# Kernel optimization log

Measured on AMD Instinct MI355X. Metric: run time of the kernel, lower is better.

## Reference

```python
import jax, jax.numpy as jnp
import numpy as np

DIM = 1024
HEADS = 16
HD = DIM // HEADS  # 64
EPS = 1.1920928955078125e-07  # torch.finfo(float32).eps, RMSNorm default


def setup_inputs() -> dict:
    key = jax.random.key(0)
    ks = jax.random.split(key, 8)
    s = 0.02
    return {
        "x": jax.random.normal(ks[0], (2, 2048, DIM), jnp.float32),
        "pe": jax.random.normal(ks[1], (1, 1, 2048, HD // 2, 2, 2), jnp.float32),
        "qkv_w": jax.random.normal(ks[2], (3 * DIM, DIM), jnp.float32) * s,
        "qkv_b": jax.random.normal(ks[3], (3 * DIM,), jnp.float32) * s,
        "q_norm_w": jnp.ones((HD,), jnp.float32),
        "k_norm_w": jnp.ones((HD,), jnp.float32),
        "proj_w": jax.random.normal(ks[4], (DIM, DIM), jnp.float32) * s,
        "proj_b": jax.random.normal(ks[5], (DIM,), jnp.float32) * s,
    }


def _rms_norm(t, w):
    var = jnp.mean(jnp.square(t), axis=-1, keepdims=True)
    return t * jax.lax.rsqrt(var + EPS) * w


def _apply_rope(t, pe):
    # t: [B,H,L,D]; pe: [1,1,L,D/2,2,2]
    B, H, L, D = t.shape
    tp = t.reshape(B, H, L, D // 2, 1, 2)
    out = pe[..., 0] * tp[..., 0] + pe[..., 1] * tp[..., 1]  # [B,H,L,D/2,2]
    return out.reshape(B, H, L, D)


def reference(x, pe, qkv_w, qkv_b, q_norm_w, k_norm_w, proj_w, proj_b):
    B, L, _ = x.shape
    qkv = x @ qkv_w.T + qkv_b  # [B,L,3*DIM]
    qkv = qkv.reshape(B, L, 3, HEADS, HD).transpose(2, 0, 3, 1, 4)  # [3,B,H,L,D]
    q, k, v = qkv[0], qkv[1], qkv[2]
    q = _rms_norm(q, q_norm_w)
    k = _rms_norm(k, k_norm_w)
    q = _apply_rope(q, pe)
    k = _apply_rope(k, pe)
    scale = 1.0 / np.sqrt(HD).astype(np.float32)
    scores = jnp.einsum("bhqd,bhkd->bhqk", q, k) * scale  # [B,H,L,L]
    attn = jax.nn.softmax(scores, axis=-1)
    o = jnp.einsum("bhqk,bhkd->bhqd", attn, v)  # [B,H,L,D]
    o = o.transpose(0, 2, 1, 3).reshape(B, L, DIM)  # B L (H D)
    return o @ proj_w.T + proj_b
```

## Files before the change

kernel.cpp:

```cpp
#include <hip/hip_runtime.h>
#include <hip/hip_bf16.h>

#define DIM   1024
#define HEADS 16
#define HD    64
#define BB    2
#define LL    2048
#define MTOT  (BB*LL)
#define EPSV  1.1920928955078125e-07f

typedef __attribute__((ext_vector_type(8))) short bf16x8;
typedef __attribute__((ext_vector_type(4))) float f32x4;
typedef unsigned short ushort_t;

__device__ __forceinline__ float bf2f(ushort_t u) {
    unsigned int x = ((unsigned int)u) << 16;
    return __builtin_bit_cast(float, x);
}
__device__ __forceinline__ ushort_t f2bf(float f) {
    unsigned int x = __builtin_bit_cast(unsigned int, f);
    unsigned int r = (x + 0x7FFFu + ((x >> 16) & 1u)) >> 16;
    return (ushort_t)r;
}

__global__ __launch_bounds__(256) void f32_to_bf16_k(const float* __restrict__ in,
                                                     ushort_t* __restrict__ out, int n) {
    int i = (blockIdx.x * 256 + threadIdx.x) * 4;
    if (i < n) {
        float4 v = *(const float4*)(in + i);
        ushort4 o;
        o.x = f2bf(v.x); o.y = f2bf(v.y); o.z = f2bf(v.z); o.w = f2bf(v.w);
        *(ushort4*)(out + i) = o;
    }
}

template <int OUT_BF16>
__global__ __launch_bounds__(256) void gemm_bt(const ushort_t* __restrict__ A,
                                               const ushort_t* __restrict__ Bt,
                                               const float* __restrict__ bias,
                                               void* __restrict__ Cout,
                                               int M, int N, int K) {
    __shared__ __attribute__((aligned(16))) ushort_t Asm[128 * 32];
    __shared__ __attribute__((aligned(16))) ushort_t Bsm[128 * 32];
    int tid = threadIdx.x;
    int lane = tid & 63, wid = tid >> 6;
    int wm = wid >> 1, wn = wid & 1;
    int r = lane & 15, g = lane >> 4;
    int m0 = blockIdx.y * 128, n0 = blockIdx.x * 128;

    f32x4 acc[4][4] = {};

    int niter = K >> 5;
    for (int kk = 0; kk < niter; ++kk) {
        int k0 = kk << 5;
        __syncthreads();
#pragma unroll
        for (int p = 0; p < 2; ++p) {
            int off = (p * 256 + tid) * 8;
            int row = off >> 5, col = off & 31;
            int ldsoff = (p * 256 + wid * 64) * 8;
            __builtin_amdgcn_global_load_lds(
                (const __attribute__((address_space(1))) void*)(A + (size_t)(m0 + row) * K + k0 + col),
                (__attribute__((address_space(3))) void*)(Asm + ldsoff), 16, 0, 0);
            __builtin_amdgcn_global_load_lds(
                (const __attribute__((address_space(1))) void*)(Bt + (size_t)(n0 + row) * K + k0 + col),
                (__attribute__((address_space(3))) void*)(Bsm + ldsoff), 16, 0, 0);
        }
        __syncthreads();
        bf16x8 af[4], bfr[4];
#pragma unroll
        for (int mi = 0; mi < 4; mi++)
            af[mi] = *(const bf16x8*)(Asm + (wm * 64 + mi * 16 + r) * 32 + g * 8);
#pragma unroll
        for (int ni = 0; ni < 4; ni++)
            bfr[ni] = *(const bf16x8*)(Bsm + (wn * 64 + ni * 16 + r) * 32 + g * 8);
#pragma unroll
        for (int mi = 0; mi < 4; mi++)
#pragma unroll
            for (int ni = 0; ni < 4; ni++)
                acc[mi][ni] = __builtin_amdgcn_mfma_f32_16x16x32_bf16(af[mi], bfr[ni], acc[mi][ni], 0, 0, 0);
    }
#pragma unroll
    for (int mi = 0; mi < 4; mi++)
#pragma unroll
        for (int ni = 0; ni < 4; ni++) {
            int col = n0 + wn * 64 + ni * 16 + r;
            float bv = bias[col];
#pragma unroll
            for (int reg = 0; reg < 4; reg++) {
                int row = m0 + wm * 64 + mi * 16 + g * 4 + reg;
                float v = acc[mi][ni][reg] + bv;
                if (OUT_BF16)
                    ((ushort_t*)Cout)[(size_t)row * N + col] = f2bf(v);
                else
                    ((float*)Cout)[(size_t)row * N + col] = v;
            }
        }
}

__global__ __launch_bounds__(256) void norm_rope_k(const ushort_t* __restrict__ qkv,
                                                   const float* __restrict__ pe,
                                                   const float* __restrict__ qnw,
                                                   const float* __restrict__ knw,
                                                   ushort_t* __restrict__ qh,
                                                   ushort_t* __restrict__ kh,
                                                   ushort_t* __restrict__ vT) {
    __shared__ ushort_t T[64][68];
    const int tid = threadIdx.x;
    const int lane = tid & 63, w = tid >> 6;
    const int rg = lane >> 4;
    const int d4 = (lane & 15) * 4;
    const int l0 = blockIdx.x * 64;
    const int t  = blockIdx.y;
    const int bh = blockIdx.z;
    const int b = bh >> 4, h = bh & 15;

    if (t == 2) {
#pragma unroll
        for (int i = 0; i < 4; ++i) {
            int ll = w * 16 + rg + 4 * i;
            int m = b * 2048 + l0 + ll;
            ushort4 v = *(const ushort4*)(qkv + (size_t)m * 3072 + 2048 + h * 64 + d4);
            *(ushort4*)(&T[ll][d4]) = v;
        }
        __syncthreads();
        const int d = tid >> 2, lq = (tid & 3) * 16;
        ushort_t* dst = vT + ((size_t)(bh * 64 + d)) * 2048 + l0 + lq;
#pragma unroll
        for (int c = 0; c < 4; ++c) {
            ushort4 o;
            o.x = T[lq + c * 4 + 0][d];
            o.y = T[lq + c * 4 + 1][d];
            o.z = T[lq + c * 4 + 2][d];
            o.w = T[lq + c * 4 + 3][d];
            *(ushort4*)(dst + c * 4) = o;
        }
        return;
    }

    const float* nwp = (t == 0) ? qnw : knw;
    const float4 nwv = *(const float4*)(nwp + d4);
    ushort_t* dst = (t == 0) ? qh : kh;
    const float qscale = (t == 0) ? 0.125f : 1.0f;
#pragma unroll
    for (int i = 0; i < 4; ++i) {
        int ll = w * 16 + rg + 4 * i;
        int l = l0 + ll;
        int m = b * 2048 + l;
        ushort4 vv = *(const ushort4*)(qkv + (size_t)m * 3072 + t * 1024 + h * 64 + d4);
        float v0 = bf2f(vv.x), v1 = bf2f(vv.y), v2 = bf2f(vv.z), v3 = bf2f(vv.w);
        float ss = v0 * v0 + v1 * v1 + v2 * v2 + v3 * v3;
        ss += __shfl_xor(ss, 1, 64);
        ss += __shfl_xor(ss, 2, 64);
        ss += __shfl_xor(ss, 4, 64);
        ss += __shfl_xor(ss, 8, 64);
        float rms = rsqrtf(ss * (1.0f / 64.0f) + EPSV);
        v0 *= rms * nwv.x; v1 *= rms * nwv.y; v2 *= rms * nwv.z; v3 *= rms * nwv.w;
        float4 p0 = *(const float4*)(pe + (size_t)l * 128 + 2 * d4);
        float4 p1 = *(const float4*)(pe + (size_t)l * 128 + 2 * d4 + 4);
        float o0 = (p0.x * v0 + p0.y * v1) * qscale;
        float o1 = (p0.z * v0 + p0.w * v1) * qscale;
        float o2 = (p1.x * v2 + p1.y * v3) * qscale;
        float o3 = (p1.z * v2 + p1.w * v3) * qscale;
        ushort4 o;
        o.x = f2bf(o0); o.y = f2bf(o1); o.z = f2bf(o2); o.w = f2bf(o3);
        *(ushort4*)(dst + ((size_t)bh * 2048 + l) * 64 + d4) = o;
    }
}

__global__ __launch_bounds__(256, 2) void attn_k(const ushort_t* __restrict__ qh,
                                                 const ushort_t* __restrict__ kh,
                                                 const ushort_t* __restrict__ vT,
                                                 ushort_t* __restrict__ ob) {
    __shared__ __attribute__((aligned(16))) ushort_t Ksm[2][64 * 64];
    __shared__ __attribute__((aligned(16))) ushort_t Vsm[2][64 * 64];
    __shared__ __attribute__((aligned(16))) ushort_t Plds[4][2][16 * 64];

    const int tid = threadIdx.x;
    const int lane = tid & 63, wid = tid >> 6;
    const int r = lane & 15, g = lane >> 4;
    const int qt = blockIdx.x, bh = blockIdx.y;
    const int q0 = qt * 128 + wid * 32;
    const ushort_t* Q  = qh + (size_t)bh * LL * 64;
    const ushort_t* Kb = kh + (size_t)bh * LL * 64;
    const ushort_t* Vt = vT + (size_t)bh * 64 * LL;

    int row_[2], ccx_[2];
#pragma unroll
    for (int q = 0; q < 2; ++q) {
        int c = q * 256 + tid;
        row_[q] = c >> 3;
        ccx_[q] = (c & 7) ^ (row_[q] & 7);
    }
    const int swz = (r & 7) * 8;

    bf16x8 qf[2][2];
#pragma unroll
    for (int mf = 0; mf < 2; ++mf)
#pragma unroll
        for (int hf = 0; hf < 2; ++hf)
            qf[mf][hf] = *(const bf16x8*)(Q + (size_t)(q0 + mf * 16 + r) * 64 + hf * 32 + g * 8);

    f32x4 acc[2][4] = {};
    float mrow[2] = {-1e30f, -1e30f};
    float srow[2] = {0.f, 0.f};
    const f32x4 zero = {};

#pragma unroll
    for (int q = 0; q < 2; ++q) {
        __builtin_amdgcn_global_load_lds(
            (const __attribute__((address_space(1))) void*)(Kb + (size_t)row_[q] * 64 + ccx_[q] * 8),
            (__attribute__((address_space(3))) void*)(&Ksm[0][0] + (q * 256 + wid * 64) * 8), 16, 0, 0);
        __builtin_amdgcn_global_load_lds(
            (const __attribute__((address_space(1))) void*)(Vt + (size_t)row_[q] * 2048 + ccx_[q] * 8),
            (__attribute__((address_space(3))) void*)(&Vsm[0][0] + (q * 256 + wid * 64) * 8), 16, 0, 0);
    }
    __syncthreads();

    int buf = 0;
    for (int it = 0; it < 32; ++it) {
        if (it < 31) {
            int kvn = (it + 1) * 64;
#pragma unroll
            for (int q = 0; q < 2; ++q) {
                __builtin_amdgcn_global_load_lds(
                    (const __attribute__((address_space(1))) void*)(Kb + (size_t)(kvn + row_[q]) * 64 + ccx_[q] * 8),
                    (__attribute__((address_space(3))) void*)(&Ksm[buf ^ 1][0] + (q * 256 + wid * 64) * 8), 16, 0, 0);
                __builtin_amdgcn_global_load_lds(
                    (const __attribute__((address_space(1))) void*)(Vt + (size_t)row_[q] * 2048 + kvn + ccx_[q] * 8),
                    (__attribute__((address_space(3))) void*)(&Vsm[buf ^ 1][0] + (q * 256 + wid * 64) * 8), 16, 0, 0);
            }
        }
        const ushort_t* Kl = &Ksm[buf][0];
        const ushort_t* Vl = &Vsm[buf][0];

        bf16x8 kf[4][2];
#pragma unroll
        for (int kt = 0; kt < 4; ++kt)
#pragma unroll
            for (int hf = 0; hf < 2; ++hf)
                kf[kt][hf] = *(const bf16x8*)(Kl + (kt * 16 + r) * 64 + (((hf * 4 + g) * 8) ^ swz));

        f32x4 s[2][4];
        __builtin_amdgcn_s_setprio(1);
#pragma unroll
        for (int mf = 0; mf < 2; ++mf)
#pragma unroll
            for (int kt = 0; kt < 4; ++kt) {
                f32x4 t0 = __builtin_amdgcn_mfma_f32_16x16x32_bf16(kf[kt][0], qf[mf][0], zero, 0, 0, 0);
                s[mf][kt] = __builtin_amdgcn_mfma_f32_16x16x32_bf16(kf[kt][1], qf[mf][1], t0, 0, 0, 0);
            }
        __builtin_amdgcn_s_setprio(0);

#pragma unroll
        for (int mf = 0; mf < 2; ++mf) {
            float pm = -1e30f;
#pragma unroll
            for (int kt = 0; kt < 4; ++kt)
#pragma unroll
                for (int reg = 0; reg < 4; ++reg) pm = fmaxf(pm, s[mf][kt][reg]);
            pm = fmaxf(pm, __shfl_xor(pm, 16, 64));
            pm = fmaxf(pm, __shfl_xor(pm, 32, 64));
            bool skip = (__all(pm <= mrow[mf] + 8.0f) != 0);
            float mn, al;
            if (skip) {
                mn = mrow[mf];
            } else {
                mn = fmaxf(mrow[mf], pm);
                al = __expf(mrow[mf] - mn);
                mrow[mf] = mn;
            }
            float rs = 0.f;
#pragma unroll
            for (int kt = 0; kt < 4; ++kt)
#pragma unroll
                for (int reg = 0; reg < 4; ++reg) {
                    float p = __expf(s[mf][kt][reg] - mn);
                    s[mf][kt][reg] = p;
                    rs += p;
                }
            rs += __shfl_xor(rs, 16, 64);
            rs += __shfl_xor(rs, 32, 64);
            if (skip) {
                srow[mf] += rs;
            } else {
                srow[mf] = srow[mf] * al + rs;
                float ab[4];
#pragma unroll
                for (int reg = 0; reg < 4; ++reg) ab[reg] = __shfl(al, g * 4 + reg, 16);
#pragma unroll
                for (int dt = 0; dt < 4; ++dt)
#pragma unroll
                    for (int reg = 0; reg < 4; ++reg) acc[mf][dt][reg] *= ab[reg];
            }
#pragma unroll
            for (int kt = 0; kt < 4; ++kt) {
                ushort4 pw;
                pw.x = f2bf(s[mf][kt][0]); pw.y = f2bf(s[mf][kt][1]);
                pw.z = f2bf(s[mf][kt][2]); pw.w = f2bf(s[mf][kt][3]);
                *(ushort4*)(&Plds[wid][mf][0] + r * 64 + (((2 * kt + (g >> 1)) * 8) ^ swz) + (g & 1) * 4) = pw;
            }
        }
        asm volatile("s_waitcnt lgkmcnt(0)" ::: "memory");
        __builtin_amdgcn_sched_barrier(0);

        bf16x8 pa[2][2];
#pragma unroll
        for (int mf = 0; mf < 2; ++mf)
#pragma unroll
            for (int hf = 0; hf < 2; ++hf)
                pa[mf][hf] = *(const bf16x8*)(&Plds[wid][mf][0] + r * 64 + (((hf * 4 + g) * 8) ^ swz));

        __builtin_amdgcn_s_setprio(1);
#pragma unroll
        for (int dt = 0; dt < 4; ++dt)
#pragma unroll
            for (int hv = 0; hv < 2; ++hv) {
                bf16x8 vf = *(const bf16x8*)(Vl + (dt * 16 + r) * 64 + (((hv * 4 + g) * 8) ^ swz));
#pragma unroll
                for (int mf = 0; mf < 2; ++mf)
                    acc[mf][dt] = __builtin_amdgcn_mfma_f32_16x16x32_bf16(pa[mf][hv], vf, acc[mf][dt], 0, 0, 0);
            }
        __builtin_amdgcn_s_setprio(0);

        __syncthreads();
        buf ^= 1;
    }

    int b = bh >> 4, h = bh & 15;
#pragma unroll
    for (int mf = 0; mf < 2; ++mf) {
        float sinv = 1.0f / srow[mf];
        float sb[4];
#pragma unroll
        for (int reg = 0; reg < 4; ++reg) sb[reg] = __shfl(sinv, g * 4 + reg, 16);
#pragma unroll
        for (int dt = 0; dt < 4; ++dt)
#pragma unroll
            for (int reg = 0; reg < 4; ++reg) {
                int l = q0 + mf * 16 + g * 4 + reg;
                ob[((size_t)(b * 2048 + l)) * 1024 + h * 64 + dt * 16 + r] =
                    f2bf(acc[mf][dt][reg] * sb[reg]);
            }
    }
}

extern "C" void kernel_launch(void* const* d_in, const int* in_sizes, int n_in,
                              void* d_out, int out_size, void* d_ws, size_t ws_size,
                              hipStream_t stream) {
    const float* x      = (const float*)d_in[0];
    const float* pe     = (const float*)d_in[1];
    const float* qkv_w  = (const float*)d_in[2];
    const float* qkv_b  = (const float*)d_in[3];
    const float* qnw    = (const float*)d_in[4];
    const float* knw    = (const float*)d_in[5];
    const float* proj_w = (const float*)d_in[6];
    const float* proj_b = (const float*)d_in[7];
    float* out = (float*)d_out;

    char* ws = (char*)d_ws;
    ushort_t* xb    = (ushort_t*)(ws);
    ushort_t* wqkv  = (ushort_t*)(ws + 8388608);
    ushort_t* wproj = (ushort_t*)(ws + 8388608 + 6291456);
    ushort_t* qkvb  = (ushort_t*)(ws + 16777216);
    ushort_t* qhp   = (ushort_t*)(ws + 16777216 + 25165824);
    ushort_t* khp   = (ushort_t*)(ws + 16777216 + 25165824 + 8388608);
    ushort_t* vtp   = (ushort_t*)(ws + 16777216 + 25165824 + 2 * 8388608);
    ushort_t* obp   = qkvb;

    f32_to_bf16_k<<<MTOT * DIM / 1024, 256, 0, stream>>>(x, xb, MTOT * DIM);
    f32_to_bf16_k<<<3 * DIM * DIM / 1024, 256, 0, stream>>>(qkv_w, wqkv, 3 * DIM * DIM);
    f32_to_bf16_k<<<DIM * DIM / 1024, 256, 0, stream>>>(proj_w, wproj, DIM * DIM);

    gemm_bt<1><<<dim3(3 * DIM / 128, MTOT / 128), 256, 0, stream>>>(xb, wqkv, qkv_b, qkvb,
                                                                    MTOT, 3 * DIM, DIM);
    norm_rope_k<<<dim3(32, 3, 32), 256, 0, stream>>>(qkvb, pe, qnw, knw, qhp, khp, vtp);
    attn_k<<<dim3(16, 32), 256, 0, stream>>>(qhp, khp, vtp, obp);
    gemm_bt<0><<<dim3(DIM / 128, MTOT / 128), 256, 0, stream>>>(obp, wproj, proj_b, out,
                                                                MTOT, DIM, DIM);
}
```

Measured before the change: 232.7 us.

## Replace QKV GEMM with 256x256-tile double-buffered direct-to-LDS kernel

Adds a new bf16 GEMM for the QKV projection. It uses 256x256 output tiles, 512 threads and a 64-wide K step. Global loads go straight into LDS through global_load_lds, with an XOR-swizzled layout and double buffering to overlap the next tile's load with MFMA work. A block-index swizzle groups tiles for L2 locality, and s_setprio is raised around the MFMA loop. The larger tiles increase data reuse per block, but the grid drops to 192 blocks, fewer than the CU count. About 128KB of LDS per block also limits each CU to one block.

```diff
diff --git a/kernel.cpp b/kernel.cpp
--- a/kernel.cpp
+++ b/kernel.cpp
@@ -31,6 +31,112 @@
         ushort4 o;
         o.x = f2bf(v.x); o.y = f2bf(v.y); o.z = f2bf(v.z); o.w = f2bf(v.w);
         *(ushort4*)(out + i) = o;
+    }
+}
+
+__global__ __launch_bounds__(512, 2) void gemm256(const ushort_t* __restrict__ A,
+                                                  const ushort_t* __restrict__ Bt,
+                                                  const float* __restrict__ bias,
+                                                  ushort_t* __restrict__ C,
+                                                  int M, int N, int K) {
+    __shared__ __attribute__((aligned(16))) ushort_t Asm[2][256 * 64];
+    __shared__ __attribute__((aligned(16))) ushort_t Bsm[2][256 * 64];
+    const int tid = threadIdx.x;
+    const int lane = tid & 63, wid = tid >> 6;
+    const int wm = wid >> 1, wn = wid & 1;
+    const int r = lane & 15, g = lane >> 4;
+
+    const int mtiles = M >> 8;
+    const int cpx = gridDim.x >> 3;
+    const int bid = blockIdx.x;
+    const int swz = (bid & 7) * cpx + (bid >> 3);
+    const int mt = swz % mtiles, nt = swz / mtiles;
+    const int m0 = mt * 256, n0 = nt * 256;
+
+    int srow[2], sgx[2];
+#pragma unroll
+    for (int q = 0; q < 2; ++q) {
+        int c = q * 512 + tid;
+        srow[q] = c >> 3;
+        sgx[q] = ((c & 7) ^ (srow[q] & 7)) * 8;
+    }
+    const ushort_t* pa[2][2];
+    const ushort_t* pb[2][2];
+#pragma unroll
+    for (int q = 0; q < 2; ++q)
+#pragma unroll
+        for (int h = 0; h < 2; ++h) {
+            pa[q][h] = A + (size_t)(m0 + h * 128 + srow[q]) * K + sgx[q];
+            pb[q][h] = Bt + (size_t)(n0 + h * 128 + srow[q]) * K + sgx[q];
+        }
+
+    f32x4 acc[4][8] = {};
+
+    auto stage = [&](int kt, int slot) {
+        const int kc = kt * 64;
+#pragma unroll
+        for (int h = 0; h < 2; ++h)
+#pragma unroll
+            for (int q = 0; q < 2; ++q) {
+                __builtin_amdgcn_global_load_lds(
+                    (const __attribute__((address_space(1))) void*)(pa[q][h] + kc),
+                    (__attribute__((address_space(3))) void*)(&Asm[slot][0] + h * 8192 + (q * 512 + wid * 64) * 8),
+                    16, 0, 0);
+                __builtin_amdgcn_global_load_lds(
+                    (const __attribute__((address_space(1))) void*)(pb[q][h] + kc),
+                    (__attribute__((address_space(3))) void*)(&Bsm[slot][0] + h * 8192 + (q * 512 + wid * 64) * 8),
+                    16, 0, 0);
+            }
+    };
+
+    stage(0, 0);
+    asm volatile("s_waitcnt vmcnt(0)" ::: "memory");
+    __builtin_amdgcn_s_barrier();
+    asm volatile("" ::: "memory");
+
+    const int nkt = K >> 6;
+    for (int kt = 0; kt < nkt; ++kt) {
+        const int slot = kt & 1;
+        if (kt + 1 < nkt) stage(kt + 1, slot ^ 1);
+        const ushort_t* As = &Asm[slot][0];
+        const ushort_t* Bs = &Bsm[slot][0];
+#pragma unroll
+        for (int ks = 0; ks < 2; ++ks) {
+            bf16x8 af[4], bf[8];
+#pragma unroll
+            for (int mi = 0; mi < 4; ++mi) {
+                int row = wm * 64 + mi * 16 + r;
+                af[mi] = *(const bf16x8*)(As + row * 64 + (((ks * 4 + g) * 8) ^ ((row & 7) * 8)));
+            }
+#pragma unroll
+            for (int ni = 0; ni < 8; ++ni) {
+                int row = wn * 128 + ni * 16 + r;
+                bf[ni] = *(const bf16x8*)(Bs + row * 64 + (((ks * 4 + g) * 8) ^ ((row & 7) * 8)));
+            }
+            __builtin_amdgcn_s_setprio(1);
+#pragma unroll
+            for (int mi = 0; mi < 4; ++mi)
+#pragma unroll
+                for (int ni = 0; ni < 8; ++ni)
+                    acc[mi][ni] = __builtin_amdgcn_mfma_f32_16x16x32_bf16(af[mi], bf[ni], acc[mi][ni], 0, 0, 0);
+            __builtin_amdgcn_s_setprio(0);
+        }
+        asm volatile("s_waitcnt vmcnt(0)" ::: "memory");
+        __builtin_amdgcn_s_barrier();
+        asm volatile("" ::: "memory");
+    }
+
+#pragma unroll
+    for (int ni = 0; ni < 8; ++ni) {
+        int col = n0 + wn * 128 + ni * 16 + r;
+        float bv = bias[col];
+#pragma unroll
+        for (int mi = 0; mi < 4; ++mi)
+#pragma unroll
+            for (int reg = 0; reg < 4; ++reg) {
+                int row = m0 + wm * 64 + mi * 16 + g * 4 + reg;
+                C[(size_t)row * N + col] = f2bf(acc[mi][ni][reg] + bv);
+            }
     }
 }
 
@@ -372,8 +478,8 @@
     f32_to_bf16_k<<<3 * DIM * DIM / 1024, 256, 0, stream>>>(qkv_w, wqkv, 3 * DIM * DIM);
     f32_to_bf16_k<<<DIM * DIM / 1024, 256, 0, stream>>>(proj_w, wproj, DIM * DIM);
 
-    gemm_bt<1><<<dim3(3 * DIM / 128, MTOT / 128), 256, 0, stream>>>(xb, wqkv, qkv_b, qkvb,
-                                                                    MTOT, 3 * DIM, DIM);
+    gemm256<<<(MTOT / 256) * (3 * DIM / 256), 512, 0, stream>>>(xb, wqkv, qkv_b, qkvb,
+                                                                MTOT, 3 * DIM, DIM);
     norm_rope_k<<<dim3(32, 3, 32), 256, 0, stream>>>(qkvb, pe, qnw, knw, qhp, khp, vtp);
     attn_k<<<dim3(16, 32), 256, 0, stream>>>(qhp, khp, vtp, obp);
     gemm_bt<0><<<dim3(DIM / 128, MTOT / 128), 256, 0, stream>>>(obp, wproj, proj_b, out,
```

Result: no change. 234.6 us (+0.8%).
